# Performance work log

Hardware: AMD Instinct MI355X
Metric: run time of the kernel (lower is better)

The kernel has to match this reference:

```python
import jax, jax.numpy as jnp
import numpy as np

PIXEL_SIZE = 0.1
PI = 3.141592653589793


def setup_inputs() -> dict:
    key = jax.random.key(0)
    batch = jax.random.normal(key, (128, 1, 512, 512), dtype=jnp.float32)
    return {"batch": batch}


def _hann_window(roi):
    # lin = linspace(-roi/2, roi/2, roi); r[i,j] = sqrt(lin[j]^2 + lin[i]^2)
    lin = jnp.linspace(-roi / 2, roi / 2, roi, dtype=jnp.float32)
    r = jnp.sqrt(lin[None, :] ** 2 + lin[:, None] ** 2)
    hann = 0.5 * (1.0 + jnp.cos(PI * r / (roi / 2)))
    hann = jnp.where(r > roi / 2, 0.0, hann)
    return hann  # [roi, roi]


def _radial_segments(roi, n_freq):
    # radialDst = round(sqrt(xx^2 + yy^2)) with x = arange(-cx, roi-cx)
    cx = roi // 2
    x = np.arange(-cx, roi - cx, dtype=np.float64)
    xx, yy = np.meshgrid(x, x, indexing="ij")
    rad = np.round(np.sqrt(xx ** 2 + yy ** 2)).astype(np.int32)
    # bins >= n_freq go into an overflow segment that is discarded
    seg = np.where(rad < n_freq, rad, n_freq)
    return jnp.asarray(seg.ravel())


def reference(batch):
    px = PIXEL_SIZE
    roi = batch.shape[-1]
    cx = roi // 2
    n_freq = cx + 1
    nyquist = 1.0 / (2.0 * px)

    # subtract per-ROI mean
    batch_nm = batch - jnp.mean(batch, axis=(2, 3), keepdims=True)

    # Hann-windowed 2D power spectrum, averaged over realizations
    hann = _hann_window(roi)[None, None, :, :]
    F = jnp.fft.fftshift(jnp.fft.fft2(batch_nm * hann, axes=(2, 3)), axes=(2, 3))
    ps = jnp.mean(jnp.abs(F) ** 2, axis=0)            # [1, roi, roi]
    nps2D = (px ** 2 / roi ** 2) * jnp.squeeze(ps)    # [roi, roi]

    # single-pass radial mean binning (replaces per-k boolean-mask loop)
    seg = _radial_segments(roi, n_freq)
    flat = nps2D.ravel()
    sums = jax.ops.segment_sum(flat, seg, num_segments=n_freq + 1)[:n_freq]
    counts = jax.ops.segment_sum(jnp.ones_like(flat), seg, num_segments=n_freq + 1)[:n_freq]
    nps1D = sums / counts

    f1D = jnp.linspace(0.0, nyquist, n_freq, dtype=jnp.float32)
    return nps1D, nps2D, f1D
```

## Files before the change

### kernel.cpp

```cpp
#include <hip/hip_runtime.h>

#define N 512
#define NF 257
#define NB 128
#define PI_F 3.14159265358979323846f
#define C_SQ2 0.70710678118654752440f

__device__ __forceinline__ float2 cmul(float2 a, float2 b) {
    return make_float2(a.x * b.x - a.y * b.y, a.x * b.y + a.y * b.x);
}
__device__ __forceinline__ void bf(float2& a, float2& b) {
    float2 t = b;
    b = make_float2(a.x - t.x, a.y - t.y);
    a = make_float2(a.x + t.x, a.y + t.y);
}
__device__ __forceinline__ void bf_tw(float2& a, float2& b, float2 w) {
    float2 t = cmul(b, w);
    b = make_float2(a.x - t.x, a.y - t.y);
    a = make_float2(a.x + t.x, a.y + t.y);
}
__device__ __forceinline__ void bf_ni(float2& a, float2& b) {
    float2 t = make_float2(b.y, -b.x);
    b = make_float2(a.x - t.x, a.y - t.y);
    a = make_float2(a.x + t.x, a.y + t.y);
}
__device__ __forceinline__ void lds_fence() {
    asm volatile("s_waitcnt lgkmcnt(0)" ::: "memory");
}

__device__ __forceinline__ void fft512(float2 v[8], float* lre, float* lim, int l) {
    const float2 w64  = make_float2(C_SQ2, -C_SQ2);
    const float2 w192 = make_float2(-C_SQ2, -C_SQ2);
    bf(v[0], v[1]); bf(v[2], v[3]); bf(v[4], v[5]); bf(v[6], v[7]);
    bf(v[0], v[2]); bf_ni(v[1], v[3]); bf(v[4], v[6]); bf_ni(v[5], v[7]);
    bf(v[0], v[4]); bf_tw(v[1], v[5], w64); bf_ni(v[2], v[6]); bf_tw(v[3], v[7], w192);
#pragma unroll
    for (int e = 0; e < 8; e++) { lre[9 * l + e] = v[e].x; lim[9 * l + e] = v[e].y; }
    lds_fence();
    int g = l >> 3, r = l & 7;
#pragma unroll
    for (int t = 0; t < 8; t++) {
        int p = 72 * g + 9 * t + r;
        v[t].x = lre[p]; v[t].y = lim[p];
    }
    float sn, cs;
    __sincosf(-(PI_F / 32.0f) * (float)r, &sn, &cs);
    float2 W1 = make_float2(cs, sn);
    float2 W2 = cmul(W1, W1);
    float2 W3 = cmul(W2, W2);
    float2 W2n = make_float2(W2.y, -W2.x);
    bf_tw(v[0], v[1], W3); bf_tw(v[2], v[3], W3); bf_tw(v[4], v[5], W3); bf_tw(v[6], v[7], W3);
    bf_tw(v[0], v[2], W2); bf_tw(v[1], v[3], W2n); bf_tw(v[4], v[6], W2); bf_tw(v[5], v[7], W2n);
    {
        float2 W1a = cmul(W1, w64);
        float2 W1n = make_float2(W1.y, -W1.x);
        float2 W1c = cmul(W1, w192);
        bf_tw(v[0], v[4], W1); bf_tw(v[1], v[5], W1a); bf_tw(v[2], v[6], W1n); bf_tw(v[3], v[7], W1c);
    }
#pragma unroll
    for (int t = 0; t < 8; t++) {
        int p = 72 * g + 9 * t + r;
        lre[p] = v[t].x; lim[p] = v[t].y;
    }
    lds_fence();
#pragma unroll
    for (int t = 0; t < 8; t++) {
        int p = 72 * t + l + (l >> 3);
        v[t].x = lre[p]; v[t].y = lim[p];
    }
    __sincosf(-(PI_F / 256.0f) * (float)l, &sn, &cs);
    float2 Wc = make_float2(cs, sn);
    float2 w2 = cmul(Wc, Wc);
    float2 w4 = cmul(w2, w2);
    float2 w2n = make_float2(w2.y, -w2.x);
    bf_tw(v[0], v[1], w4); bf_tw(v[2], v[3], w4); bf_tw(v[4], v[5], w4); bf_tw(v[6], v[7], w4);
    bf_tw(v[0], v[2], w2); bf_tw(v[1], v[3], w2n); bf_tw(v[4], v[6], w2); bf_tw(v[5], v[7], w2n);
    {
        float2 Wca = cmul(Wc, w64);
        float2 Wcn = make_float2(Wc.y, -Wc.x);
        float2 Wcc = cmul(Wc, w192);
        bf_tw(v[0], v[4], Wc); bf_tw(v[1], v[5], Wca); bf_tw(v[2], v[6], Wcn); bf_tw(v[3], v[7], Wcc);
    }
}

__global__ void zero_kernel(float* __restrict__ acc, float* __restrict__ bins,
                            float* __restrict__ meanacc) {
    int i = blockIdx.x * blockDim.x + threadIdx.x;
    if (i < N * N) acc[i] = 0.0f;
    if (i < 2 * (NF + 1)) bins[i] = 0.0f;
    if (i < NB) meanacc[i] = 0.0f;
}

__global__ __launch_bounds__(512) void hannfft_kernel(float2* __restrict__ Hrow) {
    __shared__ float sm[9216];
    int tid = threadIdx.x;
    int w = tid >> 6, l = tid & 63;
    int rowbase = blockIdx.x << 4;
    int r1 = rowbase + 2 * w, r2 = r1 + 1;

    const float step = (float)N / (float)(N - 1);
    float a1 = -0.5f * (float)N + (float)r1 * step;
    float a2 = -0.5f * (float)N + (float)r2 * step;
    float a1s = a1 * a1, a2s = a2 * a2;

    float2 v[8];
    int rl = __brev((unsigned)l) >> 26;
#pragma unroll
    for (int e = 0; e < 8; e++) {
        int src = (int)((__brev((unsigned)e) >> 29) << 6) + rl;
        float lc = -0.5f * (float)N + (float)src * step;
        float lc2 = lc * lc;
        float rr1 = sqrtf(a1s + lc2), rr2 = sqrtf(a2s + lc2);
        float h1 = (rr1 > 256.0f) ? 0.0f : 0.5f * (1.0f + cosf(PI_F * rr1 * (1.0f / 256.0f)));
        float h2 = (rr2 > 256.0f) ? 0.0f : 0.5f * (1.0f + cosf(PI_F * rr2 * (1.0f / 256.0f)));
        v[e].x = h1;
        v[e].y = h2;
    }

    float* lre = sm + w * 1152;
    float* lim = lre + 576;
    fft512(v, lre, lim, l);
    __syncthreads();

    float* tre = sm;
    float* tim = sm + 4240;
    int lr0 = 2 * w, lr1 = lr0 + 1;
    int sl = (64 - l) & 63;
#pragma unroll
    for (int t = 0; t <= 4; t++) {
        float2 a = v[7 - t];
        float zfx = __shfl(a.x, sl);
        float zfy = __shfl(a.y, sl);
        if (l == 0) { float2 o = v[(8 - t) & 7]; zfx = o.x; zfy = o.y; }
        float2 z = v[t];
        int col = 64 * t + l;
        if (col < NF) {
            tre[lr0 * 265 + col] = 0.5f * (z.x + zfx);
            tim[lr0 * 265 + col] = 0.5f * (z.y - zfy);
            tre[lr1 * 265 + col] = 0.5f * (z.y + zfy);
            tim[lr1 * 265 + col] = 0.5f * (zfx - z.x);
        }
    }
    __syncthreads();

    int c0 = tid >> 4, rr = tid & 15;
#pragma unroll
    for (int it = 0; it < 9; it++) {
        int c = it * 32 + c0;
        if (c < NF) {
            float2 val = make_float2(tre[rr * 265 + c], tim[rr * 265 + c]);
            Hrow[(size_t)c * N + rowbase + rr] = val;
        }
    }
}

__global__ __launch_bounds__(512) void rowfft_kernel(const float* __restrict__ x,
                                                     float* __restrict__ meanacc,
                                                     float2* __restrict__ inter) {
    __shared__ float sm[9216];
    __shared__ float redsum[8];
    int tid = threadIdx.x;
    int w = tid >> 6, l = tid & 63;
    int img = blockIdx.x >> 5;
    int rowbase = (blockIdx.x & 31) << 4;
    int r1 = rowbase + 2 * w, r2 = r1 + 1;
    const float* x1 = x + ((size_t)img * N + r1) * N;
    const float* x2 = x1 + N;

    const float step = (float)N / (float)(N - 1);
    float a1 = -0.5f * (float)N + (float)r1 * step;
    float a2 = -0.5f * (float)N + (float)r2 * step;
    float a1s = a1 * a1, a2s = a2 * a2;

    float2 v[8];
    float rsum = 0.0f;
    int rl = __brev((unsigned)l) >> 26;
#pragma unroll
    for (int e = 0; e < 8; e++) {
        int src = (int)((__brev((unsigned)e) >> 29) << 6) + rl;
        float lc = -0.5f * (float)N + (float)src * step;
        float lc2 = lc * lc;
        float rr1 = sqrtf(a1s + lc2), rr2 = sqrtf(a2s + lc2);
        float h1 = (rr1 > 256.0f) ? 0.0f : 0.5f * (1.0f + __cosf(rr1 * (PI_F / 256.0f)));
        float h2 = (rr2 > 256.0f) ? 0.0f : 0.5f * (1.0f + __cosf(rr2 * (PI_F / 256.0f)));
        float xv1 = x1[src], xv2 = x2[src];
        rsum += xv1 + xv2;
        v[e].x = xv1 * h1;
        v[e].y = xv2 * h2;
    }
#pragma unroll
    for (int off = 32; off > 0; off >>= 1) rsum += __shfl_down(rsum, off);
    if (l == 0) redsum[w] = rsum;

    float* lre = sm + w * 1152;
    float* lim = lre + 576;
    fft512(v, lre, lim, l);
    __syncthreads();
    if (tid == 0) {
        float s = 0.0f;
#pragma unroll
        for (int i = 0; i < 8; i++) s += redsum[i];
        atomicAdd(meanacc + img, s);
    }

    float* tre = sm;
    float* tim = sm + 4240;
    int lr0 = 2 * w, lr1 = lr0 + 1;
    int sl = (64 - l) & 63;
#pragma unroll
    for (int t = 0; t <= 4; t++) {
        float2 a = v[7 - t];
        float zfx = __shfl(a.x, sl);
        float zfy = __shfl(a.y, sl);
        if (l == 0) { float2 o = v[(8 - t) & 7]; zfx = o.x; zfy = o.y; }
        float2 z = v[t];
        int col = 64 * t + l;
        if (col < NF) {
            tre[lr0 * 265 + col] = 0.5f * (z.x + zfx);
            tim[lr0 * 265 + col] = 0.5f * (z.y - zfy);
            tre[lr1 * 265 + col] = 0.5f * (z.y + zfy);
            tim[lr1 * 265 + col] = 0.5f * (zfx - z.x);
        }
    }
    __syncthreads();

    int c0 = tid >> 4, rr = tid & 15;
#pragma unroll
    for (int it = 0; it < 9; it++) {
        int c = it * 32 + c0;
        if (c < NF) {
            float2 val = make_float2(tre[rr * 265 + c], tim[rr * 265 + c]);
            inter[((size_t)img * NF + c) * N + rowbase + rr] = val;
        }
    }
}

__global__ __launch_bounds__(256) void colfft_kernel(const float2* __restrict__ inter,
                                                     const float2* __restrict__ Hrow,
                                                     const float* __restrict__ meanacc,
                                                     float* __restrict__ accT) {
    __shared__ float sm[4608];
    int tid = threadIdx.x;
    int w = tid >> 6, l = tid & 63;
    int col = blockIdx.x * 4 + w;
    int colc = col < NF ? col : NF - 1;
    int b0 = blockIdx.y * 8;
    float* lre = sm + w * 1152;
    float* lim = lre + 576;
    int rl = __brev((unsigned)l) >> 26;

    int off[8];
#pragma unroll
    for (int e = 0; e < 8; e++)
        off[e] = (int)((__brev((unsigned)e) >> 29) << 6) + rl;

    float2 hv[8];
    const float2* hbase = Hrow + (size_t)colc * N;
#pragma unroll
    for (int e = 0; e < 8; e++) hv[e] = hbase[off[e]];

    float pw[8];
#pragma unroll
    for (int t = 0; t < 8; t++) pw[t] = 0.0f;

    float2 nv[8];
    const float2* base0 = inter + ((size_t)b0 * NF + colc) * N;
#pragma unroll
    for (int e = 0; e < 8; e++) nv[e] = base0[off[e]];

    for (int bi = 0; bi < 8; bi++) {
        float mn = meanacc[b0 + bi] * (1.0f / ((float)N * (float)N));
        float2 v[8];
#pragma unroll
        for (int e = 0; e < 8; e++)
            v[e] = make_float2(nv[e].x - mn * hv[e].x, nv[e].y - mn * hv[e].y);
        if (bi < 7) {
            const float2* nb = inter + ((size_t)(b0 + bi + 1) * NF + colc) * N;
#pragma unroll
            for (int e = 0; e < 8; e++) nv[e] = nb[off[e]];
        }
        fft512(v, lre, lim, l);
#pragma unroll
        for (int t = 0; t < 8; t++)
            pw[t] += v[t].x * v[t].x + v[t].y * v[t].y;
    }

    if (col < NF) {
        int sv = (col + 256) & 511;
#pragma unroll
        for (int t = 0; t < 8; t++) {
            int k = 64 * t + l;
            int su = (k + 256) & 511;
            atomicAdd(&accT[(size_t)sv * N + su], pw[t]);
        }
        if (col >= 1 && col <= 255) {
            int sv2 = (768 - col) & 511;
#pragma unroll
            for (int t = 0; t < 8; t++) {
                int k = 64 * t + l;
                int su2 = (768 - k) & 511;
                atomicAdd(&accT[(size_t)sv2 * N + su2], pw[t]);
            }
        }
    }
}

__global__ __launch_bounds__(256) void finalize2d_kernel(const float* __restrict__ accT,
                                                         float* __restrict__ out2d,
                                                         float* __restrict__ bins) {
    __shared__ float lsum[NF];
    __shared__ float lcnt[NF];
    int t = threadIdx.x;
    for (int i = t; i < NF; i += 256) { lsum[i] = 0.0f; lcnt[i] = 0.0f; }
    __syncthreads();
    const float scale = (0.1f * 0.1f) / ((float)N * (float)N) / (float)NB;
    int idx = blockIdx.x * 256 + t;
    int stride = gridDim.x * 256;
    for (int q = idx; q < N * N; q += stride) {
        int j = q >> 9, i = q & (N - 1);
        float v = accT[q] * scale;
        out2d[(size_t)i * N + j] = v;
        float xi = (float)(i - N / 2), yj = (float)(j - N / 2);
        int rad = (int)rintf(sqrtf(xi * xi + yj * yj));
        if (rad < NF) {
            atomicAdd(&lsum[rad], v);
            atomicAdd(&lcnt[rad], 1.0f);
        }
    }
    __syncthreads();
    for (int i = t; i < NF; i += 256) {
        if (lsum[i] != 0.0f || lcnt[i] != 0.0f) {
            atomicAdd(&bins[i], lsum[i]);
            atomicAdd(&bins[NF + 1 + i], lcnt[i]);
        }
    }
}

__global__ void finalize1d_kernel(const float* __restrict__ bins, float* __restrict__ out) {
    int t = blockIdx.x * blockDim.x + threadIdx.x;
    if (t < NF) {
        out[t] = bins[t] / bins[NF + 1 + t];
        out[NF + N * N + t] = (float)t * (5.0f / 256.0f);
    }
}

extern "C" void kernel_launch(void* const* d_in, const int* in_sizes, int n_in,
                              void* d_out, int out_size, void* d_ws, size_t ws_size,
                              hipStream_t stream) {
    const float* x = (const float*)d_in[0];
    float* out = (float*)d_out;
    char* ws = (char*)d_ws;

    float* accT    = (float*)ws;
    float* meanacc = (float*)(ws + (size_t)N * N * sizeof(float));
    float* bins    = meanacc + NB;
    size_t off_h = (size_t)N * N * sizeof(float) + NB * sizeof(float)
                   + 2 * (NF + 1) * sizeof(float);
    off_h = (off_h + 255) & ~(size_t)255;
    float2* Hrow = (float2*)(ws + off_h);
    size_t off_inter = off_h + (size_t)NF * N * sizeof(float2);
    off_inter = (off_inter + 255) & ~(size_t)255;
    float2* inter = (float2*)(ws + off_inter);

    zero_kernel<<<dim3((N * N + 255) / 256), dim3(256), 0, stream>>>(accT, bins, meanacc);
    hannfft_kernel<<<dim3(32), dim3(512), 0, stream>>>(Hrow);
    rowfft_kernel<<<dim3(NB * 32), dim3(512), 0, stream>>>(x, meanacc, inter);
    colfft_kernel<<<dim3(65, 16), dim3(256), 0, stream>>>(inter, Hrow, meanacc, accT);
    finalize2d_kernel<<<dim3(256), dim3(256), 0, stream>>>(accT, out + NF, bins);
    finalize1d_kernel<<<dim3(2), dim3(256), 0, stream>>>(bins, out);
}
```

Measured before the change: 276.5 us.

## Store row-FFT intermediate as fp16 and precompute Hann window table

The row-FFT intermediate buffer is now stored as half2 instead of float2, which halves the global memory traffic between the row and column FFT kernels. The shared-memory staging tile uses half2 as well. A new kernel precomputes the 512x512 Hann window into a table once per call, and the row FFT kernels read it instead of evaluating sqrt and cos per element. The fp16 intermediate costs precision in the spectrum values and could affect accuracy tolerance.

```diff
diff --git a/kernel.cpp b/kernel.cpp
--- a/kernel.cpp
+++ b/kernel.cpp
@@ -1,4 +1,5 @@
 #include <hip/hip_runtime.h>
+#include <hip/hip_fp16.h>
 
 #define N 512
 #define NF 257
@@ -91,30 +92,34 @@
     if (i < NB) meanacc[i] = 0.0f;
 }
 
-__global__ __launch_bounds__(512) void hannfft_kernel(float2* __restrict__ Hrow) {
+__global__ __launch_bounds__(256) void hanntab_kernel(float* __restrict__ htab) {
+    int i = blockIdx.x * 256 + threadIdx.x;
+    int r = i >> 9, c = i & (N - 1);
+    const float step = (float)N / (float)(N - 1);
+    float a = -0.5f * (float)N + (float)r * step;
+    float b = -0.5f * (float)N + (float)c * step;
+    float rr = sqrtf(a * a + b * b);
+    float h = (rr > 256.0f) ? 0.0f : 0.5f * (1.0f + cosf(rr * (PI_F / 256.0f)));
+    htab[i] = h;
+}
+
+__global__ __launch_bounds__(512) void hannfft_kernel(const float* __restrict__ htab,
+                                                      float2* __restrict__ Hrow) {
     __shared__ float sm[9216];
     int tid = threadIdx.x;
     int w = tid >> 6, l = tid & 63;
     int rowbase = blockIdx.x << 4;
     int r1 = rowbase + 2 * w, r2 = r1 + 1;
-
-    const float step = (float)N / (float)(N - 1);
-    float a1 = -0.5f * (float)N + (float)r1 * step;
-    float a2 = -0.5f * (float)N + (float)r2 * step;
-    float a1s = a1 * a1, a2s = a2 * a2;
+    const float* h1row = htab + (size_t)r1 * N;
+    const float* h2row = htab + (size_t)r2 * N;
 
     float2 v[8];
     int rl = __brev((unsigned)l) >> 26;
 #pragma unroll
     for (int e = 0; e < 8; e++) {
         int src = (int)((__brev((unsigned)e) >> 29) << 6) + rl;
-        float lc = -0.5f * (float)N + (float)src * step;
-        float lc2 = lc * lc;
-        float rr1 = sqrtf(a1s + lc2), rr2 = sqrtf(a2s + lc2);
-        float h1 = (rr1 > 256.0f) ? 0.0f : 0.5f * (1.0f + cosf(PI_F * rr1 * (1.0f / 256.0f)));
-        float h2 = (rr2 > 256.0f) ? 0.0f : 0.5f * (1.0f + cosf(PI_F * rr2 * (1.0f / 256.0f)));
-        v[e].x = h1;
-        v[e].y = h2;
+        v[e].x = h1row[src];
+        v[e].y = h2row[src];
     }
 
     float* lre = sm + w * 1152;
@@ -155,8 +160,9 @@
 }
 
 __global__ __launch_bounds__(512) void rowfft_kernel(const float* __restrict__ x,
+                                                     const float* __restrict__ htab,
                                                      float* __restrict__ meanacc,
-                                                     float2* __restrict__ inter) {
+                                                     __half2* __restrict__ inter) {
     __shared__ float sm[9216];
     __shared__ float redsum[8];
     int tid = threadIdx.x;
@@ -166,11 +172,8 @@
     int r1 = rowbase + 2 * w, r2 = r1 + 1;
     const float* x1 = x + ((size_t)img * N + r1) * N;
     const float* x2 = x1 + N;
-
-    const float step = (float)N / (float)(N - 1);
-    float a1 = -0.5f * (float)N + (float)r1 * step;
-    float a2 = -0.5f * (float)N + (float)r2 * step;
-    float a1s = a1 * a1, a2s = a2 * a2;
+    const float* h1row = htab + (size_t)r1 * N;
+    const float* h2row = htab + (size_t)r2 * N;
 
     float2 v[8];
     float rsum = 0.0f;
@@ -178,15 +181,10 @@
 #pragma unroll
     for (int e = 0; e < 8; e++) {
         int src = (int)((__brev((unsigned)e) >> 29) << 6) + rl;
-        float lc = -0.5f * (float)N + (float)src * step;
-        float lc2 = lc * lc;
-        float rr1 = sqrtf(a1s + lc2), rr2 = sqrtf(a2s + lc2);
-        float h1 = (rr1 > 256.0f) ? 0.0f : 0.5f * (1.0f + __cosf(rr1 * (PI_F / 256.0f)));
-        float h2 = (rr2 > 256.0f) ? 0.0f : 0.5f * (1.0f + __cosf(rr2 * (PI_F / 256.0f)));
         float xv1 = x1[src], xv2 = x2[src];
         rsum += xv1 + xv2;
-        v[e].x = xv1 * h1;
-        v[e].y = xv2 * h2;
+        v[e].x = xv1 * h1row[src];
+        v[e].y = xv2 * h2row[src];
     }
 #pragma unroll
     for (int off = 32; off > 0; off >>= 1) rsum += __shfl_down(rsum, off);
@@ -203,8 +201,7 @@
         atomicAdd(meanacc + img, s);
     }
 
-    float* tre = sm;
-    float* tim = sm + 4240;
+    __half2* tile = (__half2*)sm;
     int lr0 = 2 * w, lr1 = lr0 + 1;
     int sl = (64 - l) & 63;
 #pragma unroll
@@ -216,10 +213,8 @@
         float2 z = v[t];
         int col = 64 * t + l;
         if (col < NF) {
-            tre[lr0 * 265 + col] = 0.5f * (z.x + zfx);
-            tim[lr0 * 265 + col] = 0.5f * (z.y - zfy);
-            tre[lr1 * 265 + col] = 0.5f * (z.y + zfy);
-            tim[lr1 * 265 + col] = 0.5f * (zfx - z.x);
+            tile[lr0 * 265 + col] = __floats2half2_rn(0.5f * (z.x + zfx), 0.5f * (z.y - zfy));
+            tile[lr1 * 265 + col] = __floats2half2_rn(0.5f * (z.y + zfy), 0.5f * (zfx - z.x));
         }
     }
     __syncthreads();
@@ -229,13 +224,12 @@
     for (int it = 0; it < 9; it++) {
         int c = it * 32 + c0;
         if (c < NF) {
-            float2 val = make_float2(tre[rr * 265 + c], tim[rr * 265 + c]);
-            inter[((size_t)img * NF + c) * N + rowbase + rr] = val;
-        }
-    }
-}
-
-__global__ __launch_bounds__(256) void colfft_kernel(const float2* __restrict__ inter,
+            inter[((size_t)img * NF + c) * N + rowbase + rr] = tile[rr * 265 + c];
+        }
+    }
+}
+
+__global__ __launch_bounds__(256) void colfft_kernel(const __half2* __restrict__ inter,
                                                      const float2* __restrict__ Hrow,
                                                      const float* __restrict__ meanacc,
                                                      float* __restrict__ accT) {
@@ -263,8 +257,8 @@
 #pragma unroll
     for (int t = 0; t < 8; t++) pw[t] = 0.0f;
 
-    float2 nv[8];
-    const float2* base0 = inter + ((size_t)b0 * NF + colc) * N;
+    __half2 nv[8];
+    const __half2* base0 = inter + ((size_t)b0 * NF + colc) * N;
 #pragma unroll
     for (int e = 0; e < 8; e++) nv[e] = base0[off[e]];
 
@@ -272,10 +266,12 @@
         float mn = meanacc[b0 + bi] * (1.0f / ((float)N * (float)N));
         float2 v[8];
 #pragma unroll
-        for (int e = 0; e < 8; e++)
-            v[e] = make_float2(nv[e].x - mn * hv[e].x, nv[e].y - mn * hv[e].y);
+        for (int e = 0; e < 8; e++) {
+            float2 z = __half22float2(nv[e]);
+            v[e] = make_float2(z.x - mn * hv[e].x, z.y - mn * hv[e].y);
+        }
         if (bi < 7) {
-            const float2* nb = inter + ((size_t)(b0 + bi + 1) * NF + colc) * N;
+            const __half2* nb = inter + ((size_t)(b0 + bi + 1) * NF + colc) * N;
 #pragma unroll
             for (int e = 0; e < 8; e++) nv[e] = nb[off[e]];
         }
@@ -358,13 +354,17 @@
                    + 2 * (NF + 1) * sizeof(float);
     off_h = (off_h + 255) & ~(size_t)255;
     float2* Hrow = (float2*)(ws + off_h);
-    size_t off_inter = off_h + (size_t)NF * N * sizeof(float2);
+    size_t off_t = off_h + (size_t)NF * N * sizeof(float2);
+    off_t = (off_t + 255) & ~(size_t)255;
+    float* htab = (float*)(ws + off_t);
+    size_t off_inter = off_t + (size_t)N * N * sizeof(float);
     off_inter = (off_inter + 255) & ~(size_t)255;
-    float2* inter = (float2*)(ws + off_inter);
+    __half2* inter = (__half2*)(ws + off_inter);
 
     zero_kernel<<<dim3((N * N + 255) / 256), dim3(256), 0, stream>>>(accT, bins, meanacc);
-    hannfft_kernel<<<dim3(32), dim3(512), 0, stream>>>(Hrow);
-    rowfft_kernel<<<dim3(NB * 32), dim3(512), 0, stream>>>(x, meanacc, inter);
+    hanntab_kernel<<<dim3(N * N / 256), dim3(256), 0, stream>>>(htab);
+    hannfft_kernel<<<dim3(32), dim3(512), 0, stream>>>(htab, Hrow);
+    rowfft_kernel<<<dim3(NB * 32), dim3(512), 0, stream>>>(x, htab, meanacc, inter);
     colfft_kernel<<<dim3(65, 16), dim3(256), 0, stream>>>(inter, Hrow, meanacc, accT);
     finalize2d_kernel<<<dim3(256), dim3(256), 0, stream>>>(accT, out + NF, bins);
     finalize1d_kernel<<<dim3(2), dim3(256), 0, stream>>>(bins, out);
```

Result: faster. 270.4 us (-2.2%).
